# Kernel optimization log

Hardware: AMD Instinct MI355X
Metric: run time of the kernel (lower is better)

## Reference

```python
import jax, jax.numpy as jnp
import numpy as np

N_NODES = 100000
N_EDGES = 1600000
D_IN = 256
D_OUT = 128


def setup_inputs() -> dict:
    key = jax.random.key(0)
    k1, k2, k3, k4, k5 = jax.random.split(key, 5)
    x = jax.random.normal(k1, (N_NODES, D_IN), dtype=jnp.float32)
    # Glorot-uniform weight as in weight_variable_glorot
    init_range = np.sqrt(6.0 / (D_IN + D_OUT))
    W = jax.random.uniform(k2, (D_IN, D_OUT), dtype=jnp.float32,
                           minval=-init_range, maxval=init_range)
    adj_rows = jax.random.randint(k3, (N_EDGES,), 0, N_NODES, dtype=jnp.int32)
    adj_cols = jax.random.randint(k4, (N_EDGES,), 0, N_NODES, dtype=jnp.int32)
    adj_vals = jax.random.uniform(k5, (N_EDGES,), dtype=jnp.float32)
    return {"x": x, "W": W, "adj_rows": adj_rows, "adj_cols": adj_cols,
            "adj_vals": adj_vals}


def reference(x, W, adj_rows, adj_cols, adj_vals):
    # dropout with keep_prob = 1 - 0.0 is the identity -> omitted
    h = x @ W                                    # [N, D_OUT] dense projection
    # sparse (COO) adjacency @ h : out[r] += v * h[c]
    msgs = adj_vals[:, None] * h[adj_cols]       # [E, D_OUT]
    agg = jax.ops.segment_sum(msgs, adj_rows, num_segments=N_NODES)
    return jax.nn.relu(agg)                      # act = tf.nn.relu
```

## Files before the change

kernel.cpp:

```cpp
#include <hip/hip_runtime.h>
#include <hip/hip_bf16.h>

#define N_NODES 100000
#define N_EDGES 1600000
#define D_IN 256
#define D_OUT 128
#define CAP 64

typedef short bf16x8 __attribute__((ext_vector_type(8)));
typedef float f32x4 __attribute__((ext_vector_type(4)));
typedef float f32x2 __attribute__((ext_vector_type(2)));

__device__ __forceinline__ unsigned short f2bf(float f) {
    unsigned int u = __builtin_bit_cast(unsigned int, f);
    u += 0x7fffu + ((u >> 16) & 1u);
    return (unsigned short)(u >> 16);
}
__device__ __forceinline__ float bf_lo(unsigned int h) {
    return __builtin_bit_cast(float, h << 16);
}
__device__ __forceinline__ float bf_hi(unsigned int h) {
    return __builtin_bit_cast(float, h & 0xffff0000u);
}

__global__ __launch_bounds__(256) void convert_w(const float* __restrict__ W,
                                                 unsigned short* __restrict__ WbT,
                                                 int* __restrict__ cursor,
                                                 int bucket_mode) {
    int i = blockIdx.x * 256 + threadIdx.x;
    int k = i >> 7;
    int n = i & 127;
    WbT[(size_t)n * D_IN + k] = f2bf(W[i]);
    int z = i * 4;
    if (z < N_NODES) {
        int4 v = bucket_mode ? make_int4(z << 6, (z << 6) + CAP, (z << 6) + 2 * CAP, (z << 6) + 3 * CAP)
                             : make_int4(0, 0, 0, 0);
        *(int4*)(cursor + z) = v;
    }
}

#define GEMM_BLOCKS ((N_NODES + 63) / 64)
__global__ __launch_bounds__(256) void gemm_mfma(const float* __restrict__ x,
                                                 const unsigned short* __restrict__ WbT,
                                                 unsigned short* __restrict__ hb) {
    const int wave = threadIdx.x >> 6;
    const int lane = threadIdx.x & 63;
    const int row0 = blockIdx.x * 64 + wave * 16;
    if (row0 >= N_NODES) return;
    const int m = lane & 15;
    const int q = lane >> 4;

    const float* xr = x + (size_t)(row0 + m) * D_IN + q * 8;

    float4 a[8][2];
#pragma unroll
    for (int kc = 0; kc < 8; ++kc) {
        a[kc][0] = *(const float4*)(xr + kc * 32);
        a[kc][1] = *(const float4*)(xr + kc * 32 + 4);
    }

    bf16x8 af[8];
#pragma unroll
    for (int kc = 0; kc < 8; ++kc) {
        af[kc][0] = (short)f2bf(a[kc][0].x); af[kc][1] = (short)f2bf(a[kc][0].y);
        af[kc][2] = (short)f2bf(a[kc][0].z); af[kc][3] = (short)f2bf(a[kc][0].w);
        af[kc][4] = (short)f2bf(a[kc][1].x); af[kc][5] = (short)f2bf(a[kc][1].y);
        af[kc][6] = (short)f2bf(a[kc][1].z); af[kc][7] = (short)f2bf(a[kc][1].w);
    }

    f32x4 acc[8];
#pragma unroll
    for (int nt = 0; nt < 8; ++nt) acc[nt] = (f32x4){0.f, 0.f, 0.f, 0.f};

#pragma unroll
    for (int kc = 0; kc < 8; ++kc) {
        const int kb = kc * 32 + q * 8;
#pragma unroll
        for (int nt = 0; nt < 8; ++nt) {
            bf16x8 bf = *(const bf16x8*)(WbT + (size_t)(nt * 16 + m) * D_IN + kb);
            acc[nt] = __builtin_amdgcn_mfma_f32_16x16x32_bf16(af[kc], bf, acc[nt], 0, 0, 0);
        }
    }

#pragma unroll
    for (int nt = 0; nt < 8; ++nt)
#pragma unroll
        for (int r = 0; r < 4; ++r) {
            int grow = row0 + q * 4 + r;
            hb[(size_t)grow * D_OUT + nt * 16 + m] = f2bf(acc[nt][r]);
        }
}

#define NWIN 16
#define ROWS_PER_WIN (N_NODES / NWIN)
#define PERM_SLICES 250
__global__ __launch_bounds__(256) void scatter_bucket(const int* __restrict__ rows,
                                                      const int* __restrict__ cols,
                                                      const float* __restrict__ vals,
                                                      int* __restrict__ cursor,
                                                      int2* __restrict__ buckets) {
    const int w8    = blockIdx.x & 7;
    const int slice = blockIdx.x >> 3;
    const int per = (N_EDGES / 4) / PERM_SLICES;
    const int beg = slice * per;
    const int end = beg + per;
#pragma unroll
    for (int ph = 0; ph < 2; ++ph) {
        const int lo = (w8 + ph * 8) * ROWS_PER_WIN;
        const int hi = lo + ROWS_PER_WIN;
        for (int i = beg + (int)threadIdx.x; i < end; i += 256) {
            int4 r = *((const int4*)rows + i);
            const int e = i * 4;
            if (r.x >= lo && r.x < hi) {
                int p = atomicAdd(&cursor[r.x], 1);
                buckets[p] = make_int2(cols[e + 0], __builtin_bit_cast(int, vals[e + 0]));
            }
            if (r.y >= lo && r.y < hi) {
                int p = atomicAdd(&cursor[r.y], 1);
                buckets[p] = make_int2(cols[e + 1], __builtin_bit_cast(int, vals[e + 1]));
            }
            if (r.z >= lo && r.z < hi) {
                int p = atomicAdd(&cursor[r.z], 1);
                buckets[p] = make_int2(cols[e + 2], __builtin_bit_cast(int, vals[e + 2]));
            }
            if (r.w >= lo && r.w < hi) {
                int p = atomicAdd(&cursor[r.w], 1);
                buckets[p] = make_int2(cols[e + 3], __builtin_bit_cast(int, vals[e + 3]));
            }
        }
    }
}

__global__ __launch_bounds__(256) void gather_bucket(const int* __restrict__ cursor,
                                                     const int2* __restrict__ buckets,
                                                     const unsigned short* __restrict__ hb,
                                                     float* __restrict__ out) {
    int row  = blockIdx.x * 4 + (threadIdx.x >> 6);
    int lane = threadIdx.x & 63;
    if (row >= N_NODES) return;
    int beg = row << 6;
    int end = __builtin_amdgcn_readfirstlane(cursor[row]);

    float ax0 = 0.f, ay0 = 0.f, ax1 = 0.f, ay1 = 0.f;
    float ax2 = 0.f, ay2 = 0.f, ax3 = 0.f, ay3 = 0.f;
    int j = beg;
    for (; j + 4 <= end; j += 4) {
        int4 p01 = *(const int4*)(buckets + j);
        int4 p23 = *(const int4*)(buckets + j + 2);
        unsigned int h0 = *(const unsigned int*)(hb + (size_t)p01.x * D_OUT + lane * 2);
        unsigned int h1 = *(const unsigned int*)(hb + (size_t)p01.z * D_OUT + lane * 2);
        unsigned int h2 = *(const unsigned int*)(hb + (size_t)p23.x * D_OUT + lane * 2);
        unsigned int h3 = *(const unsigned int*)(hb + (size_t)p23.z * D_OUT + lane * 2);
        float v0 = __builtin_bit_cast(float, p01.y);
        float v1 = __builtin_bit_cast(float, p01.w);
        float v2 = __builtin_bit_cast(float, p23.y);
        float v3 = __builtin_bit_cast(float, p23.w);
        ax0 = fmaf(v0, bf_lo(h0), ax0); ay0 = fmaf(v0, bf_hi(h0), ay0);
        ax1 = fmaf(v1, bf_lo(h1), ax1); ay1 = fmaf(v1, bf_hi(h1), ay1);
        ax2 = fmaf(v2, bf_lo(h2), ax2); ay2 = fmaf(v2, bf_hi(h2), ay2);
        ax3 = fmaf(v3, bf_lo(h3), ax3); ay3 = fmaf(v3, bf_hi(h3), ay3);
    }
    for (; j < end; ++j) {
        int2 e = buckets[j];
        unsigned int h = *(const unsigned int*)(hb + (size_t)e.x * D_OUT + lane * 2);
        float v = __builtin_bit_cast(float, e.y);
        ax0 = fmaf(v, bf_lo(h), ax0);
        ay0 = fmaf(v, bf_hi(h), ay0);
    }
    float accx = (ax0 + ax1) + (ax2 + ax3);
    float accy = (ay0 + ay1) + (ay2 + ay3);
    f32x2 o;
    o[0] = fmaxf(accx, 0.f);
    o[1] = fmaxf(accy, 0.f);
    __builtin_nontemporal_store(o, (f32x2*)(out + (size_t)row * D_OUT + lane * 2));
}

__global__ __launch_bounds__(256) void hist_rows(const int* __restrict__ rows,
                                                 int* __restrict__ counts) {
    int i = blockIdx.x * 256 + threadIdx.x;
    if (i < N_EDGES / 4) {
        int4 r = *(const int4*)(rows + i * 4);
        atomicAdd(&counts[r.x], 1);
        atomicAdd(&counts[r.y], 1);
        atomicAdd(&counts[r.z], 1);
        atomicAdd(&counts[r.w], 1);
    }
}

#define SCHUNK 1024
#define NSCAN ((N_NODES + SCHUNK - 1) / SCHUNK)
__global__ __launch_bounds__(1024) void scan_reduce(const int* __restrict__ counts,
                                                    int* __restrict__ bsum, int n) {
    __shared__ int ws[16];
    const int t = threadIdx.x, lane = t & 63, wid = t >> 6;
    int i = blockIdx.x * SCHUNK + t;
    int v = (i < n) ? counts[i] : 0;
#pragma unroll
    for (int off = 32; off >= 1; off >>= 1) v += __shfl_down(v, off);
    if (lane == 0) ws[wid] = v;
    __syncthreads();
    if (t == 0) {
        int s = 0;
#pragma unroll
        for (int w = 0; w < 16; ++w) s += ws[w];
        bsum[blockIdx.x] = s;
    }
}

__global__ __launch_bounds__(1024) void scan_apply(const int* __restrict__ counts,
                                                   const int* __restrict__ bsum,
                                                   int* __restrict__ ptr,
                                                   int* __restrict__ cursor, int n, int nb) {
    __shared__ int wtot[16];
    __shared__ int bpre[128];
    const int t = threadIdx.x, lane = t & 63, wid = t >> 6;
    int i = blockIdx.x * SCHUNK + t;
    int v = (i < n) ? counts[i] : 0;
    int x = v;
#pragma unroll
    for (int off = 1; off < 64; off <<= 1) {
        int u = __shfl_up(x, off);
        if (lane >= off) x += u;
    }
    if (lane == 63) wtot[wid] = x;

    if (wid == 0) {
        int carry = 0;
        for (int base = 0; base < nb; base += 64) {
            int idx = base + lane;
            int bv = (idx < nb) ? bsum[idx] : 0;
            int bx = bv;
#pragma unroll
            for (int off = 1; off < 64; off <<= 1) {
                int u = __shfl_up(bx, off);
                if (lane >= off) bx += u;
            }
            if (idx < nb) bpre[idx] = bx - bv + carry;
            carry += __shfl(bx, 63);
        }
    }
    __syncthreads();
    if (wid == 0) {
        int wv = (lane < 16) ? wtot[lane] : 0;
        int y = wv;
#pragma unroll
        for (int off = 1; off < 16; off <<= 1) {
            int u = __shfl_up(y, off);
            if (lane >= off) y += u;
        }
        if (lane < 16) wtot[lane] = y - wv;
    }
    __syncthreads();
    int excl = (x - v) + wtot[wid] + bpre[blockIdx.x];
    if (i < n) {
        ptr[i] = excl;
        cursor[i] = excl;
        if (i == n - 1) ptr[n] = excl + v;
    }
}

__global__ __launch_bounds__(256) void permute_edges(const int* __restrict__ rows,
                                                     const int* __restrict__ cols,
                                                     const float* __restrict__ vals,
                                                     int* __restrict__ cursor,
                                                     int2* __restrict__ edge_r) {
    const int w     = blockIdx.x & 7;
    const int slice = blockIdx.x >> 3;
    const int lo = w * (N_NODES / 8);
    const int hi = lo + (N_NODES / 8);
    const int per = (N_EDGES / 4) / PERM_SLICES;
    const int beg = slice * per;
    const int end = beg + per;
    for (int i = beg + (int)threadIdx.x; i < end; i += 256) {
        int4 r = *((const int4*)rows + i);
        const int e = i * 4;
        if (r.x >= lo && r.x < hi) {
            int p = atomicAdd(&cursor[r.x], 1);
            edge_r[p] = make_int2(cols[e + 0], __builtin_bit_cast(int, vals[e + 0]));
        }
        if (r.y >= lo && r.y < hi) {
            int p = atomicAdd(&cursor[r.y], 1);
            edge_r[p] = make_int2(cols[e + 1], __builtin_bit_cast(int, vals[e + 1]));
        }
        if (r.z >= lo && r.z < hi) {
            int p = atomicAdd(&cursor[r.z], 1);
            edge_r[p] = make_int2(cols[e + 2], __builtin_bit_cast(int, vals[e + 2]));
        }
        if (r.w >= lo && r.w < hi) {
            int p = atomicAdd(&cursor[r.w], 1);
            edge_r[p] = make_int2(cols[e + 3], __builtin_bit_cast(int, vals[e + 3]));
        }
    }
}

__global__ __launch_bounds__(256) void gather_rows(const int* __restrict__ ptr,
                                                   const int2* __restrict__ edge_r,
                                                   const unsigned short* __restrict__ hb,
                                                   float* __restrict__ out) {
    int row  = blockIdx.x * 4 + (threadIdx.x >> 6);
    int lane = threadIdx.x & 63;
    if (row >= N_NODES) return;
    int beg = __builtin_amdgcn_readfirstlane(ptr[row]);
    int end = __builtin_amdgcn_readfirstlane(ptr[row + 1]);

    float ax0 = 0.f, ay0 = 0.f, ax1 = 0.f, ay1 = 0.f;
    float ax2 = 0.f, ay2 = 0.f, ax3 = 0.f, ay3 = 0.f;
    int j = beg;
    for (; j + 4 <= end; j += 4) {
        int2 e0 = edge_r[j + 0];
        int2 e1 = edge_r[j + 1];
        int2 e2 = edge_r[j + 2];
        int2 e3 = edge_r[j + 3];
        unsigned int h0 = *(const unsigned int*)(hb + (size_t)e0.x * D_OUT + lane * 2);
        unsigned int h1 = *(const unsigned int*)(hb + (size_t)e1.x * D_OUT + lane * 2);
        unsigned int h2 = *(const unsigned int*)(hb + (size_t)e2.x * D_OUT + lane * 2);
        unsigned int h3 = *(const unsigned int*)(hb + (size_t)e3.x * D_OUT + lane * 2);
        float v0 = __builtin_bit_cast(float, e0.y);
        float v1 = __builtin_bit_cast(float, e1.y);
        float v2 = __builtin_bit_cast(float, e2.y);
        float v3 = __builtin_bit_cast(float, e3.y);
        ax0 = fmaf(v0, bf_lo(h0), ax0); ay0 = fmaf(v0, bf_hi(h0), ay0);
        ax1 = fmaf(v1, bf_lo(h1), ax1); ay1 = fmaf(v1, bf_hi(h1), ay1);
        ax2 = fmaf(v2, bf_lo(h2), ax2); ay2 = fmaf(v2, bf_hi(h2), ay2);
        ax3 = fmaf(v3, bf_lo(h3), ax3); ay3 = fmaf(v3, bf_hi(h3), ay3);
    }
    for (; j < end; ++j) {
        int2 e = edge_r[j];
        unsigned int h = *(const unsigned int*)(hb + (size_t)e.x * D_OUT + lane * 2);
        float v = __builtin_bit_cast(float, e.y);
        ax0 = fmaf(v, bf_lo(h), ax0);
        ay0 = fmaf(v, bf_hi(h), ay0);
    }
    float accx = (ax0 + ax1) + (ax2 + ax3);
    float accy = (ay0 + ay1) + (ay2 + ay3);
    float2 o = make_float2(fmaxf(accx, 0.f), fmaxf(accy, 0.f));
    *(float2*)(out + (size_t)row * D_OUT + lane * 2) = o;
}

extern "C" void kernel_launch(void* const* d_in, const int* in_sizes, int n_in,
                              void* d_out, int out_size, void* d_ws, size_t ws_size,
                              hipStream_t stream) {
    const float* x    = (const float*)d_in[0];
    const float* W    = (const float*)d_in[1];
    const int*   rows = (const int*)d_in[2];
    const int*   cols = (const int*)d_in[3];
    const float* vals = (const float*)d_in[4];
    float* out = (float*)d_out;

    char* ws = (char*)d_ws;
    size_t off = 0;
    unsigned short* hb  = (unsigned short*)(ws + off); off += ((size_t)N_NODES * D_OUT * 2 + 255) & ~(size_t)255;
    unsigned short* WbT = (unsigned short*)(ws + off); off += ((size_t)D_IN * D_OUT * 2 + 255) & ~(size_t)255;
    int*  cursor = (int*)(ws + off); off += ((size_t)N_NODES * 4 + 255) & ~(size_t)255;

    const size_t bucket_bytes = (size_t)N_NODES * CAP * 8;

    if (ws_size >= off + bucket_bytes) {
        int2* buckets = (int2*)(ws + off);
        convert_w<<<(D_IN * D_OUT) / 256, 256, 0, stream>>>(W, WbT, cursor, 1);
        gemm_mfma<<<GEMM_BLOCKS, 256, 0, stream>>>(x, WbT, hb);
        scatter_bucket<<<8 * PERM_SLICES, 256, 0, stream>>>(rows, cols, vals, cursor, buckets);
        gather_bucket<<<(N_NODES + 3) / 4, 256, 0, stream>>>(cursor, buckets, hb, out);
    } else {
        int*  ptr    = (int*)(ws + off); size_t off2 = off + (((size_t)(N_NODES + 1) * 4 + 255) & ~(size_t)255);
        int2* edge_r = (int2*)(ws + off2); off2 += ((size_t)N_EDGES * 8 + 255) & ~(size_t)255;
        int*  bsum   = (int*)(ws + off2);

        convert_w<<<(D_IN * D_OUT) / 256, 256, 0, stream>>>(W, WbT, cursor, 0);
        gemm_mfma<<<GEMM_BLOCKS, 256, 0, stream>>>(x, WbT, hb);
        hist_rows<<<(N_EDGES / 4 + 255) / 256, 256, 0, stream>>>(rows, cursor);
        scan_reduce<<<NSCAN, 1024, 0, stream>>>(cursor, bsum, N_NODES);
        scan_apply<<<NSCAN, 1024, 0, stream>>>(cursor, bsum, ptr, cursor, N_NODES, NSCAN);
        permute_edges<<<8 * PERM_SLICES, 256, 0, stream>>>(rows, cols, vals, cursor, edge_r);
        gather_rows<<<(N_NODES + 3) / 4, 256, 0, stream>>>(ptr, edge_r, hb, out);
    }
}
```

Measured before the change: 383.4 us.

## Fuse GEMM and edge bucket scatter into one launch with disjoint block roles

Merges the dense bf16 MFMA projection and the row-windowed edge scatter into a single kernel. The first blocks compute h and the remaining blocks scatter edges into per-row buckets, so the two independent phases can run concurrently and one launch boundary disappears. The scatter now uses 8 row windows in one pass per block instead of two passes over 8 of 16 windows, which doubles the window width and may change atomic and write locality. The fallback permute path now also launches 8*PERM_SLICES blocks through the NWIN macro, but that count is unchanged because NWIN became 8.

```diff
diff --git a/kernel.cpp b/kernel.cpp
--- a/kernel.cpp
+++ b/kernel.cpp
@@ -40,74 +40,26 @@
 }
 
 #define GEMM_BLOCKS ((N_NODES + 63) / 64)
-__global__ __launch_bounds__(256) void gemm_mfma(const float* __restrict__ x,
-                                                 const unsigned short* __restrict__ WbT,
-                                                 unsigned short* __restrict__ hb) {
-    const int wave = threadIdx.x >> 6;
-    const int lane = threadIdx.x & 63;
-    const int row0 = blockIdx.x * 64 + wave * 16;
-    if (row0 >= N_NODES) return;
-    const int m = lane & 15;
-    const int q = lane >> 4;
-
-    const float* xr = x + (size_t)(row0 + m) * D_IN + q * 8;
-
-    float4 a[8][2];
-#pragma unroll
-    for (int kc = 0; kc < 8; ++kc) {
-        a[kc][0] = *(const float4*)(xr + kc * 32);
-        a[kc][1] = *(const float4*)(xr + kc * 32 + 4);
-    }
-
-    bf16x8 af[8];
-#pragma unroll
-    for (int kc = 0; kc < 8; ++kc) {
-        af[kc][0] = (short)f2bf(a[kc][0].x); af[kc][1] = (short)f2bf(a[kc][0].y);
-        af[kc][2] = (short)f2bf(a[kc][0].z); af[kc][3] = (short)f2bf(a[kc][0].w);
-        af[kc][4] = (short)f2bf(a[kc][1].x); af[kc][5] = (short)f2bf(a[kc][1].y);
-        af[kc][6] = (short)f2bf(a[kc][1].z); af[kc][7] = (short)f2bf(a[kc][1].w);
-    }
-
-    f32x4 acc[8];
-#pragma unroll
-    for (int nt = 0; nt < 8; ++nt) acc[nt] = (f32x4){0.f, 0.f, 0.f, 0.f};
-
-#pragma unroll
-    for (int kc = 0; kc < 8; ++kc) {
-        const int kb = kc * 32 + q * 8;
-#pragma unroll
-        for (int nt = 0; nt < 8; ++nt) {
-            bf16x8 bf = *(const bf16x8*)(WbT + (size_t)(nt * 16 + m) * D_IN + kb);
-            acc[nt] = __builtin_amdgcn_mfma_f32_16x16x32_bf16(af[kc], bf, acc[nt], 0, 0, 0);
-        }
-    }
-
-#pragma unroll
-    for (int nt = 0; nt < 8; ++nt)
-#pragma unroll
-        for (int r = 0; r < 4; ++r) {
-            int grow = row0 + q * 4 + r;
-            hb[(size_t)grow * D_OUT + nt * 16 + m] = f2bf(acc[nt][r]);
-        }
-}
-
-#define NWIN 16
+#define NWIN 8
 #define ROWS_PER_WIN (N_NODES / NWIN)
 #define PERM_SLICES 250
-__global__ __launch_bounds__(256) void scatter_bucket(const int* __restrict__ rows,
-                                                      const int* __restrict__ cols,
-                                                      const float* __restrict__ vals,
-                                                      int* __restrict__ cursor,
-                                                      int2* __restrict__ buckets) {
-    const int w8    = blockIdx.x & 7;
-    const int slice = blockIdx.x >> 3;
-    const int per = (N_EDGES / 4) / PERM_SLICES;
-    const int beg = slice * per;
-    const int end = beg + per;
-#pragma unroll
-    for (int ph = 0; ph < 2; ++ph) {
-        const int lo = (w8 + ph * 8) * ROWS_PER_WIN;
+__global__ __launch_bounds__(256) void gemm_scatter(const float* __restrict__ x,
+                                                    const unsigned short* __restrict__ WbT,
+                                                    unsigned short* __restrict__ hb,
+                                                    const int* __restrict__ rows,
+                                                    const int* __restrict__ cols,
+                                                    const float* __restrict__ vals,
+                                                    int* __restrict__ cursor,
+                                                    int2* __restrict__ buckets) {
+    if (blockIdx.x >= GEMM_BLOCKS) {
+        const int s     = blockIdx.x - GEMM_BLOCKS;
+        const int w     = s & (NWIN - 1);
+        const int slice = s >> 3;
+        const int lo = w * ROWS_PER_WIN;
         const int hi = lo + ROWS_PER_WIN;
+        const int per = (N_EDGES / 4) / PERM_SLICES;
+        const int beg = slice * per;
+        const int end = beg + per;
         for (int i = beg + (int)threadIdx.x; i < end; i += 256) {
             int4 r = *((const int4*)rows + i);
             const int e = i * 4;
@@ -128,7 +80,55 @@
                 buckets[p] = make_int2(cols[e + 3], __builtin_bit_cast(int, vals[e + 3]));
             }
         }
-    }
+        return;
+    }
+
+    const int wave = threadIdx.x >> 6;
+    const int lane = threadIdx.x & 63;
+    const int row0 = blockIdx.x * 64 + wave * 16;
+    if (row0 >= N_NODES) return;
+    const int m = lane & 15;
+    const int q = lane >> 4;
+
+    const float* xr = x + (size_t)(row0 + m) * D_IN + q * 8;
+
+    float4 a[8][2];
+#pragma unroll
+    for (int kc = 0; kc < 8; ++kc) {
+        a[kc][0] = *(const float4*)(xr + kc * 32);
+        a[kc][1] = *(const float4*)(xr + kc * 32 + 4);
+    }
+
+    bf16x8 af[8];
+#pragma unroll
+    for (int kc = 0; kc < 8; ++kc) {
+        af[kc][0] = (short)f2bf(a[kc][0].x); af[kc][1] = (short)f2bf(a[kc][0].y);
+        af[kc][2] = (short)f2bf(a[kc][0].z); af[kc][3] = (short)f2bf(a[kc][0].w);
+        af[kc][4] = (short)f2bf(a[kc][1].x); af[kc][5] = (short)f2bf(a[kc][1].y);
+        af[kc][6] = (short)f2bf(a[kc][1].z); af[kc][7] = (short)f2bf(a[kc][1].w);
+    }
+
+    f32x4 acc[8];
+#pragma unroll
+    for (int nt = 0; nt < 8; ++nt) acc[nt] = (f32x4){0.f, 0.f, 0.f, 0.f};
+
+#pragma unroll
+    for (int kc = 0; kc < 8; ++kc) {
+        const int kb = kc * 32 + q * 8;
+#pragma unroll
+        for (int nt = 0; nt < 8; ++nt) {
+            bf16x8 bf = *(const bf16x8*)(WbT + (size_t)(nt * 16 + m) * D_IN + kb);
+            acc[nt] = __builtin_amdgcn_mfma_f32_16x16x32_bf16(af[kc], bf, acc[nt], 0, 0, 0);
+        }
+    }
+
+#pragma unroll
+    for (int nt = 0; nt < 8; ++nt)
+#pragma unroll
+        for (int r = 0; r < 4; ++r) {
+            int grow = row0 + q * 4 + r;
+            hb[(size_t)grow * D_OUT + nt * 16 + m] = f2bf(acc[nt][r]);
+        }
 }
 
 __global__ __launch_bounds__(256) void gather_bucket(const int* __restrict__ cursor,
@@ -173,6 +173,57 @@
     o[0] = fmaxf(accx, 0.f);
     o[1] = fmaxf(accy, 0.f);
     __builtin_nontemporal_store(o, (f32x2*)(out + (size_t)row * D_OUT + lane * 2));
+}
+
+__global__ __launch_bounds__(256) void gemm_mfma(const float* __restrict__ x,
+                                                 const unsigned short* __restrict__ WbT,
+                                                 unsigned short* __restrict__ hb) {
+    const int wave = threadIdx.x >> 6;
+    const int lane = threadIdx.x & 63;
+    const int row0 = blockIdx.x * 64 + wave * 16;
+    if (row0 >= N_NODES) return;
+    const int m = lane & 15;
+    const int q = lane >> 4;
+
+    const float* xr = x + (size_t)(row0 + m) * D_IN + q * 8;
+
+    float4 a[8][2];
+#pragma unroll
+    for (int kc = 0; kc < 8; ++kc) {
+        a[kc][0] = *(const float4*)(xr + kc * 32);
+        a[kc][1] = *(const float4*)(xr + kc * 32 + 4);
+    }
+
+    bf16x8 af[8];
+#pragma unroll
+    for (int kc = 0; kc < 8; ++kc) {
+        af[kc][0] = (short)f2bf(a[kc][0].x); af[kc][1] = (short)f2bf(a[kc][0].y);
+        af[kc][2] = (short)f2bf(a[kc][0].z); af[kc][3] = (short)f2bf(a[kc][0].w);
+        af[kc][4] = (short)f2bf(a[kc][1].x); af[kc][5] = (short)f2bf(a[kc][1].y);
+        af[kc][6] = (short)f2bf(a[kc][1].z); af[kc][7] = (short)f2bf(a[kc][1].w);
+    }
+
+    f32x4 acc[8];
+#pragma unroll
+    for (int nt = 0; nt < 8; ++nt) acc[nt] = (f32x4){0.f, 0.f, 0.f, 0.f};
+
+#pragma unroll
+    for (int kc = 0; kc < 8; ++kc) {
+        const int kb = kc * 32 + q * 8;
+#pragma unroll
+        for (int nt = 0; nt < 8; ++nt) {
+            bf16x8 bf = *(const bf16x8*)(WbT + (size_t)(nt * 16 + m) * D_IN + kb);
+            acc[nt] = __builtin_amdgcn_mfma_f32_16x16x32_bf16(af[kc], bf, acc[nt], 0, 0, 0);
+        }
+    }
+
+#pragma unroll
+    for (int nt = 0; nt < 8; ++nt)
+#pragma unroll
+        for (int r = 0; r < 4; ++r) {
+            int grow = row0 + q * 4 + r;
+            hb[(size_t)grow * D_OUT + nt * 16 + m] = f2bf(acc[nt][r]);
+        }
 }
 
 __global__ __launch_bounds__(256) void hist_rows(const int* __restrict__ rows,
@@ -358,8 +409,8 @@
     if (ws_size >= off + bucket_bytes) {
         int2* buckets = (int2*)(ws + off);
         convert_w<<<(D_IN * D_OUT) / 256, 256, 0, stream>>>(W, WbT, cursor, 1);
-        gemm_mfma<<<GEMM_BLOCKS, 256, 0, stream>>>(x, WbT, hb);
-        scatter_bucket<<<8 * PERM_SLICES, 256, 0, stream>>>(rows, cols, vals, cursor, buckets);
+        gemm_scatter<<<GEMM_BLOCKS + NWIN * PERM_SLICES, 256, 0, stream>>>(
+            x, WbT, hb, rows, cols, vals, cursor, buckets);
         gather_bucket<<<(N_NODES + 3) / 4, 256, 0, stream>>>(cursor, buckets, hb, out);
     } else {
         int*  ptr    = (int*)(ws + off); size_t off2 = off + (((size_t)(N_NODES + 1) * 4 + 255) & ~(size_t)255);
@@ -371,7 +422,7 @@
         hist_rows<<<(N_EDGES / 4 + 255) / 256, 256, 0, stream>>>(rows, cursor);
         scan_reduce<<<NSCAN, 1024, 0, stream>>>(cursor, bsum, N_NODES);
         scan_apply<<<NSCAN, 1024, 0, stream>>>(cursor, bsum, ptr, cursor, N_NODES, NSCAN);
-        permute_edges<<<8 * PERM_SLICES, 256, 0, stream>>>(rows, cols, vals, cursor, edge_r);
+        permute_edges<<<NWIN * PERM_SLICES, 256, 0, stream>>>(rows, cols, vals, cursor, edge_r);
         gather_rows<<<(N_NODES + 3) / 4, 256, 0, stream>>>(ptr, edge_r, hb, out);
     }
 }
```

New measurement: 375.0 us. 2.2% less time.
